# Kernel optimization log

Measured on AMD Instinct MI355X. Metric: run time of the kernel, lower is better.

## Reference

```python
import jax, jax.numpy as jnp
import numpy as np

B, S, T = 64, 512, 32
H2 = 1024          # hidden_size * 2
ATT = 512          # attention_size


def setup_inputs() -> dict:
    key = jax.random.key(0)
    k1, k2, k3, k4, k5, k6 = jax.random.split(key, 6)
    h = jax.random.normal(k1, (B, S, H2), dtype=jnp.float32)
    h_mask = jax.random.randint(k2, (B, S), 0, 2).astype(jnp.int32)
    ht = jax.random.normal(k3, (B, T, H2), dtype=jnp.float32)
    # Linear params (xavier-ish scale)
    w1_w = jax.random.normal(k4, (ATT, 2 * H2), dtype=jnp.float32) * (1.0 / np.sqrt(2 * H2))
    w1_b = jax.random.normal(k5, (ATT,), dtype=jnp.float32) * 0.02
    u_w = jax.random.normal(k6, (1, ATT), dtype=jnp.float32) * (1.0 / np.sqrt(ATT))
    return {"h": h, "h_mask": h_mask, "ht": ht, "w1_w": w1_w, "w1_b": w1_b, "u_w": u_w}


def reference(h, h_mask, ht, w1_w, w1_b, u_w):
    # h: [B,S,2H], ht: [B,T,2H], h_mask: [B,S] (1 = valid, 0 = pad)
    valid = h_mask != 0                                  # [B,S]
    ht_mean = jnp.mean(ht, axis=1, keepdims=True)        # [B,1,2H]
    h_cat = jnp.concatenate(
        [h, jnp.broadcast_to(ht_mean, h.shape)], axis=2)  # [B,S,4H]
    h_cat = jnp.where(valid[..., None], h_cat, 0.0)
    a = jnp.tanh(jnp.einsum('bsf,af->bsa', h_cat, w1_w) + w1_b)  # [B,S,ATT]
    a = jnp.where(valid[..., None], a, 0.0)
    beta = jnp.einsum('bsa,a->bs', a, u_w[0])            # [B,S]
    beta = jnp.where(valid, beta, -1e20)
    alpha = jax.nn.softmax(beta, axis=1)                 # [B,S]
    s = jnp.einsum('bs,bsd->bd', alpha, h)               # [B,2H]
    return s
```

## Files before the change

### kernel.cpp

```cpp
#include <hip/hip_runtime.h>
#include <math.h>
#include <stdint.h>

#define Bb 64
#define Ss 512
#define Tt 32
#define H2 1024
#define FF 2048
#define ATT 512
#define MM (Bb * Ss)

#define BM 64
#define BN 512
#define BK 32

typedef short bf8 __attribute__((ext_vector_type(8)));
typedef short bf4 __attribute__((ext_vector_type(4)));
typedef float f4 __attribute__((ext_vector_type(4)));

__device__ __forceinline__ unsigned short f2bf(float f) {
    unsigned u = __float_as_uint(f);
    u = (u + 0x7fffu + ((u >> 16) & 1u)) >> 16;
    return (unsigned short)u;
}

__device__ __forceinline__ void gl_lds16(const void* g, void* l) {
    __builtin_amdgcn_global_load_lds((const __attribute__((address_space(1))) void*)g,
                                     (__attribute__((address_space(3))) void*)l, 16, 0, 0);
}

__device__ __forceinline__ float tanh_fast(float x) {
    return 1.0f - 2.0f / (__expf(2.0f * x) + 1.0f);
}

__global__ void init_kernel(float* __restrict__ out) {
    int i = blockIdx.x * 256 + threadIdx.x;
    out[i] = 0.0f;
}

__global__ void mean_kernel(const float* __restrict__ ht, float* __restrict__ ht_mean) {
    int b = blockIdx.x;
    int d4 = threadIdx.x;
    const float4* p = (const float4*)(ht + (size_t)b * Tt * H2);
    float4 acc = make_float4(0.f, 0.f, 0.f, 0.f);
    #pragma unroll 4
    for (int t = 0; t < Tt; ++t) {
        float4 v = p[(size_t)t * (H2 / 4) + d4];
        acc.x += v.x; acc.y += v.y; acc.z += v.z; acc.w += v.w;
    }
    const float inv = 1.0f / (float)Tt;
    acc.x *= inv; acc.y *= inv; acc.z *= inv; acc.w *= inv;
    ((float4*)(ht_mean + (size_t)b * H2))[d4] = acc;
}

__global__ __launch_bounds__(256) void c2_kernel2(const float* __restrict__ ht_mean,
                                                  const float* __restrict__ w1_w,
                                                  const float* __restrict__ w1_b,
                                                  float* __restrict__ c2) {
    __shared__ float hm[H2];
    int b = blockIdx.x;
    for (int i = threadIdx.x; i < H2; i += 256) hm[i] = ht_mean[(size_t)b * H2 + i];
    __syncthreads();
    int a = blockIdx.y * 64 + ((int)threadIdx.x >> 2);
    int q = (int)threadIdx.x & 3;
    const float4* w   = (const float4*)(w1_w + (size_t)a * FF + H2 + q * 256);
    const float4* hm4 = (const float4*)(hm + q * 256);
    float acc = 0.f;
    #pragma unroll 8
    for (int k = 0; k < 64; ++k) {
        float4 wv = w[k]; float4 hv = hm4[k];
        acc += wv.x * hv.x + wv.y * hv.y + wv.z * hv.z + wv.w * hv.w;
    }
    acc += __shfl_xor(acc, 1);
    acc += __shfl_xor(acc, 2);
    if (q == 0) c2[(size_t)b * ATT + a] = acc + w1_b[a];
}

__global__ void convw_kernel(const float* __restrict__ w1_w, unsigned short* __restrict__ out) {
    size_t e = ((size_t)blockIdx.x * 256 + threadIdx.x) * 8;
    int row = (int)(e >> 10);
    int c = (int)(e & 1023);
    const float* src = w1_w + (size_t)row * FF + c;
    float4 a = *(const float4*)(src);
    float4 b = *(const float4*)(src + 4);
    bf8 v = { (short)f2bf(a.x), (short)f2bf(a.y), (short)f2bf(a.z), (short)f2bf(a.w),
              (short)f2bf(b.x), (short)f2bf(b.y), (short)f2bf(b.z), (short)f2bf(b.w) };
    *(bf8*)(out + e) = v;
}

__global__ __launch_bounds__(512, 4) void gemm_fused2_kernel(
        const float* __restrict__ h, const unsigned short* __restrict__ wb,
        const float* __restrict__ c2, const float* __restrict__ u_w,
        float* __restrict__ beta) {
    __shared__ __align__(16) unsigned short As[2][BM * BK];
    __shared__ __align__(16) unsigned short Bs[2][BN * BK];
    __shared__ float red[8][64];

    const int tid = (int)threadIdx.x;
    const int m0 = blockIdx.x * BM;
    const int wid = tid >> 6, lane = tid & 63;
    const int col = lane & 15, rg = lane >> 4;
    const int rswz = rg ^ ((col >> 1) & 3);

    f4 acc[4][4] = {};

    const int arow = tid >> 3;
    const int asub = tid & 7;
    const int a_elem = arow * BK + ((((asub >> 1) ^ ((arow >> 1) & 3)) * 8) + (asub & 1) * 4);
    const float* Ag = h + (size_t)(m0 + arow) * H2 + asub * 4;

    const int brow = tid >> 2;
    const int bslot_src = (tid & 3) ^ ((tid >> 3) & 3);
    const int ldsbase = wid * 512;

    #pragma unroll
    for (int c = 0; c < 4; ++c)
        gl_lds16(wb + (size_t)(c * 128 + brow) * H2 + bslot_src * 8,
                 &Bs[0][ldsbase + c * 4096]);
    {
        float4 a4 = *(const float4*)(Ag);
        bf4 ab = { (short)f2bf(a4.x), (short)f2bf(a4.y), (short)f2bf(a4.z), (short)f2bf(a4.w) };
        *(bf4*)&As[0][a_elem] = ab;
    }
    __syncthreads();

    int cur = 0;
    for (int t = 0; t < 32; ++t) {
        float4 a4n;
        if (t < 31) {
            a4n = *(const float4*)(Ag + (t + 1) * BK);
            #pragma unroll
            for (int c = 0; c < 4; ++c)
                gl_lds16(wb + (size_t)(c * 128 + brow) * H2 + (t + 1) * BK + bslot_src * 8,
                         &Bs[cur ^ 1][ldsbase + c * 4096]);
        }
        bf8 av[4], bv[4];
        #pragma unroll
        for (int i = 0; i < 4; ++i) {
            av[i] = *(const bf8*)&As[cur][(i * 16 + col) * BK + rswz * 8];
            bv[i] = *(const bf8*)&Bs[cur][(wid * 64 + i * 16 + col) * BK + rswz * 8];
        }
        #pragma unroll
        for (int i = 0; i < 4; ++i)
            #pragma unroll
            for (int j = 0; j < 4; ++j)
                acc[i][j] = __builtin_amdgcn_mfma_f32_16x16x32_bf16(av[i], bv[j], acc[i][j], 0, 0, 0);
        if (t < 31) {
            bf4 ab = { (short)f2bf(a4n.x), (short)f2bf(a4n.y), (short)f2bf(a4n.z), (short)f2bf(a4n.w) };
            *(bf4*)&As[cur ^ 1][a_elem] = ab;
        }
        __syncthreads();
        cur ^= 1;
    }

    const int b_idx = blockIdx.x >> 3;
    const float* c2b = c2 + (size_t)b_idx * ATT + wid * 64;
    const float* ub  = u_w + wid * 64;
    float rp[4][4] = {};
    #pragma unroll
    for (int j = 0; j < 4; ++j) {
        int n = j * 16 + col;
        float cv = c2b[n];
        float uv = ub[n];
        #pragma unroll
        for (int i = 0; i < 4; ++i)
            #pragma unroll
            for (int r = 0; r < 4; ++r)
                rp[i][r] += tanh_fast(acc[i][j][r] + cv) * uv;
    }
    #pragma unroll
    for (int i = 0; i < 4; ++i)
        #pragma unroll
        for (int r = 0; r < 4; ++r) {
            float v = rp[i][r];
            v += __shfl_xor(v, 1);
            v += __shfl_xor(v, 2);
            v += __shfl_xor(v, 4);
            v += __shfl_xor(v, 8);
            if (col == 0) red[wid][i * 16 + rg * 4 + r] = v;
        }
    __syncthreads();
    if (tid < 64) {
        float s = 0.f;
        #pragma unroll
        for (int w = 0; w < 8; ++w) s += red[w][tid];
        beta[(size_t)m0 + tid] = s;
    }
}

__global__ void softmax_kernel(const float* __restrict__ beta, const int* __restrict__ h_mask,
                               float* __restrict__ alpha) {
    __shared__ float red[16];
    int b = blockIdx.x;
    int s = (int)threadIdx.x;
    float v = (h_mask[(size_t)b * Ss + s] != 0) ? beta[(size_t)b * Ss + s] : -1e20f;
    float m = v;
    #pragma unroll
    for (int off = 32; off >= 1; off >>= 1) m = fmaxf(m, __shfl_xor(m, off, 64));
    int wave = s >> 6;
    if ((s & 63) == 0) red[wave] = m;
    __syncthreads();
    float mx = red[0];
    #pragma unroll
    for (int w = 1; w < 8; ++w) mx = fmaxf(mx, red[w]);
    float e = expf(v - mx);
    float sum = e;
    #pragma unroll
    for (int off = 32; off >= 1; off >>= 1) sum += __shfl_xor(sum, off, 64);
    __syncthreads();
    if ((s & 63) == 0) red[8 + wave] = sum;
    __syncthreads();
    float tot = 0.f;
    #pragma unroll
    for (int w = 0; w < 8; ++w) tot += red[8 + w];
    alpha[(size_t)b * Ss + s] = e / tot;
}

__global__ void wsum_kernel(const float* __restrict__ h, const float* __restrict__ alpha,
                            float* __restrict__ out) {
    int b = blockIdx.x;
    int d = blockIdx.y * 256 + (int)threadIdx.x;
    int s0 = blockIdx.z * 128;
    const float* hp = h + (size_t)b * Ss * H2 + (size_t)s0 * H2 + d;
    const float* ap = alpha + (size_t)b * Ss + s0;
    float acc = 0.f;
    #pragma unroll 4
    for (int s = 0; s < 128; ++s) acc = fmaf(ap[s], hp[(size_t)s * H2], acc);
    atomicAdd(&out[(size_t)b * H2 + d], acc);
}

extern "C" void kernel_launch(void* const* d_in, const int* in_sizes, int n_in,
                              void* d_out, int out_size, void* d_ws, size_t ws_size,
                              hipStream_t stream) {
    const float* h      = (const float*)d_in[0];
    const int*   h_mask = (const int*)d_in[1];
    const float* ht     = (const float*)d_in[2];
    const float* w1_w   = (const float*)d_in[3];
    const float* w1_b   = (const float*)d_in[4];
    const float* u_w    = (const float*)d_in[5];
    float* out = (float*)d_out;

    float* ws      = (float*)d_ws;
    float* ht_mean = ws;
    float* c2      = ws + 65536;
    float* beta    = ws + 98304;
    float* alpha   = ws + 131072;
    unsigned short* w1a_bf = (unsigned short*)(ws + 164864);

    hipLaunchKernelGGL(init_kernel, dim3(Bb * H2 / 256), dim3(256), 0, stream, out);
    hipLaunchKernelGGL(mean_kernel, dim3(Bb), dim3(256), 0, stream, ht, ht_mean);
    hipLaunchKernelGGL(c2_kernel2, dim3(Bb, 8), dim3(256), 0, stream, ht_mean, w1_w, w1_b, c2);
    hipLaunchKernelGGL(convw_kernel, dim3(256), dim3(256), 0, stream, w1_w, w1a_bf);
    hipLaunchKernelGGL(gemm_fused2_kernel, dim3(MM / BM), dim3(512), 0, stream,
                       h, w1a_bf, c2, u_w, beta);
    hipLaunchKernelGGL(softmax_kernel, dim3(Bb), dim3(512), 0, stream, beta, h_mask, alpha);
    hipLaunchKernelGGL(wsum_kernel, dim3(Bb, H2 / 256, 4), dim3(256), 0, stream, h, alpha, out);
}
```

Measured before the change: 294.4 us.

## Retile fused GEMM to 128x128 tiles with split-N atomic beta reduction

Replaces the 64x512 row-block GEMM (512 threads) with 128x128 output tiles on 256 threads, splitting the attention dimension across 4 workgroups. It also remaps block IDs so the N-tiles of one M-tile are spread apart, and widens the A loads to 16 floats per thread. Per-tile partial beta sums are combined with global atomicAdd instead of an in-block shared reduction, and init_kernel now zeroes beta as well. The aim is better balance between A and B reuse and more workgroups for occupancy. The cost is that each h row tile is loaded and converted 4 times, and beta picks up atomic contention.

```diff
diff --git a/kernel.cpp b/kernel.cpp
--- a/kernel.cpp
+++ b/kernel.cpp
@@ -10,12 +10,7 @@
 #define ATT 512
 #define MM (Bb * Ss)
 
-#define BM 64
-#define BN 512
-#define BK 32
-
 typedef short bf8 __attribute__((ext_vector_type(8)));
-typedef short bf4 __attribute__((ext_vector_type(4)));
 typedef float f4 __attribute__((ext_vector_type(4)));
 
 __device__ __forceinline__ unsigned short f2bf(float f) {
@@ -33,9 +28,10 @@
     return 1.0f - 2.0f / (__expf(2.0f * x) + 1.0f);
 }
 
-__global__ void init_kernel(float* __restrict__ out) {
+__global__ void init_kernel(float* __restrict__ beta, float* __restrict__ out) {
     int i = blockIdx.x * 256 + threadIdx.x;
-    out[i] = 0.0f;
+    if (i < Bb * Ss) beta[i] = 0.0f;
+    if (i < Bb * H2) out[i] = 0.0f;
 }
 
 __global__ void mean_kernel(const float* __restrict__ ht, float* __restrict__ ht_mean) {
@@ -88,57 +84,71 @@
     *(bf8*)(out + e) = v;
 }
 
-__global__ __launch_bounds__(512, 4) void gemm_fused2_kernel(
+__global__ __launch_bounds__(256, 3) void gemm_fused3_kernel(
         const float* __restrict__ h, const unsigned short* __restrict__ wb,
         const float* __restrict__ c2, const float* __restrict__ u_w,
         float* __restrict__ beta) {
-    __shared__ __align__(16) unsigned short As[2][BM * BK];
-    __shared__ __align__(16) unsigned short Bs[2][BN * BK];
-    __shared__ float red[8][64];
+    __shared__ __align__(16) unsigned short As[2][128 * 32];
+    __shared__ __align__(16) unsigned short Bs[2][128 * 32];
+
+    const int id = (int)blockIdx.x;
+    const int wg = (id & 7) * 128 + (id >> 3);
+    const int mt = wg >> 2, nt = wg & 3;
+    const int m0 = mt * 128, n0 = nt * 128;
 
     const int tid = (int)threadIdx.x;
-    const int m0 = blockIdx.x * BM;
     const int wid = tid >> 6, lane = tid & 63;
+    const int wr = (wid >> 1) * 64, wc = (wid & 1) * 64;
     const int col = lane & 15, rg = lane >> 4;
     const int rswz = rg ^ ((col >> 1) & 3);
 
     f4 acc[4][4] = {};
 
-    const int arow = tid >> 3;
-    const int asub = tid & 7;
-    const int a_elem = arow * BK + ((((asub >> 1) ^ ((arow >> 1) & 3)) * 8) + (asub & 1) * 4);
-    const float* Ag = h + (size_t)(m0 + arow) * H2 + asub * 4;
+    const int arow = tid >> 1;
+    const int ako  = (tid & 1) * 2;
+    const int aswz = (arow >> 1) & 3;
+    const float* Ag = h + (size_t)(m0 + arow) * H2 + ako * 8;
+    const int a_off0 = arow * 32 + ((ako    ) ^ aswz) * 8;
+    const int a_off1 = arow * 32 + ((ako + 1) ^ aswz) * 8;
 
     const int brow = tid >> 2;
-    const int bslot_src = (tid & 3) ^ ((tid >> 3) & 3);
-    const int ldsbase = wid * 512;
-
-    #pragma unroll
-    for (int c = 0; c < 4; ++c)
-        gl_lds16(wb + (size_t)(c * 128 + brow) * H2 + bslot_src * 8,
-                 &Bs[0][ldsbase + c * 4096]);
+    const int bsrc = (tid & 3) ^ ((tid >> 3) & 3);
+    const unsigned short* Bg = wb + (size_t)(n0 + brow) * H2 + bsrc * 8;
+    const int b_ldsbase = wid * 512;
+
+    gl_lds16(Bg,                   &Bs[0][b_ldsbase]);
+    gl_lds16(Bg + (size_t)64 * H2, &Bs[0][b_ldsbase + 2048]);
     {
-        float4 a4 = *(const float4*)(Ag);
-        bf4 ab = { (short)f2bf(a4.x), (short)f2bf(a4.y), (short)f2bf(a4.z), (short)f2bf(a4.w) };
-        *(bf4*)&As[0][a_elem] = ab;
+        float4 q0 = *(const float4*)(Ag);
+        float4 q1 = *(const float4*)(Ag + 4);
+        float4 q2 = *(const float4*)(Ag + 8);
+        float4 q3 = *(const float4*)(Ag + 12);
+        bf8 c0 = { (short)f2bf(q0.x), (short)f2bf(q0.y), (short)f2bf(q0.z), (short)f2bf(q0.w),
+                   (short)f2bf(q1.x), (short)f2bf(q1.y), (short)f2bf(q1.z), (short)f2bf(q1.w) };
+        bf8 c1 = { (short)f2bf(q2.x), (short)f2bf(q2.y), (short)f2bf(q2.z), (short)f2bf(q2.w),
+                   (short)f2bf(q3.x), (short)f2bf(q3.y), (short)f2bf(q3.z), (short)f2bf(q3.w) };
+        *(bf8*)&As[0][a_off0] = c0;
+        *(bf8*)&As[0][a_off1] = c1;
     }
     __syncthreads();
 
     int cur = 0;
     for (int t = 0; t < 32; ++t) {
-        float4 a4n;
+        float4 q0, q1, q2, q3;
         if (t < 31) {
-            a4n = *(const float4*)(Ag + (t + 1) * BK);
-            #pragma unroll
-            for (int c = 0; c < 4; ++c)
-                gl_lds16(wb + (size_t)(c * 128 + brow) * H2 + (t + 1) * BK + bslot_src * 8,
-                         &Bs[cur ^ 1][ldsbase + c * 4096]);
+            const int kn = (t + 1) * 32;
+            gl_lds16(Bg + kn,                   &Bs[cur ^ 1][b_ldsbase]);
+            gl_lds16(Bg + kn + (size_t)64 * H2, &Bs[cur ^ 1][b_ldsbase + 2048]);
+            q0 = *(const float4*)(Ag + kn);
+            q1 = *(const float4*)(Ag + kn + 4);
+            q2 = *(const float4*)(Ag + kn + 8);
+            q3 = *(const float4*)(Ag + kn + 12);
         }
         bf8 av[4], bv[4];
         #pragma unroll
         for (int i = 0; i < 4; ++i) {
-            av[i] = *(const bf8*)&As[cur][(i * 16 + col) * BK + rswz * 8];
-            bv[i] = *(const bf8*)&Bs[cur][(wid * 64 + i * 16 + col) * BK + rswz * 8];
+            av[i] = *(const bf8*)&As[cur][(wr + i * 16 + col) * 32 + rswz * 8];
+            bv[i] = *(const bf8*)&Bs[cur][(wc + i * 16 + col) * 32 + rswz * 8];
         }
         #pragma unroll
         for (int i = 0; i < 4; ++i)
@@ -146,16 +156,20 @@
             for (int j = 0; j < 4; ++j)
                 acc[i][j] = __builtin_amdgcn_mfma_f32_16x16x32_bf16(av[i], bv[j], acc[i][j], 0, 0, 0);
         if (t < 31) {
-            bf4 ab = { (short)f2bf(a4n.x), (short)f2bf(a4n.y), (short)f2bf(a4n.z), (short)f2bf(a4n.w) };
-            *(bf4*)&As[cur ^ 1][a_elem] = ab;
+            bf8 c0 = { (short)f2bf(q0.x), (short)f2bf(q0.y), (short)f2bf(q0.z), (short)f2bf(q0.w),
+                       (short)f2bf(q1.x), (short)f2bf(q1.y), (short)f2bf(q1.z), (short)f2bf(q1.w) };
+            bf8 c1 = { (short)f2bf(q2.x), (short)f2bf(q2.y), (short)f2bf(q2.z), (short)f2bf(q2.w),
+                       (short)f2bf(q3.x), (short)f2bf(q3.y), (short)f2bf(q3.z), (short)f2bf(q3.w) };
+            *(bf8*)&As[cur ^ 1][a_off0] = c0;
+            *(bf8*)&As[cur ^ 1][a_off1] = c1;
         }
         __syncthreads();
         cur ^= 1;
     }
 
-    const int b_idx = blockIdx.x >> 3;
-    const float* c2b = c2 + (size_t)b_idx * ATT + wid * 64;
-    const float* ub  = u_w + wid * 64;
+    const int b_idx = mt >> 2;
+    const float* c2b = c2 + (size_t)b_idx * ATT + n0 + wc;
+    const float* ub  = u_w + n0 + wc;
     float rp[4][4] = {};
     #pragma unroll
     for (int j = 0; j < 4; ++j) {
@@ -177,15 +191,9 @@
             v += __shfl_xor(v, 2);
             v += __shfl_xor(v, 4);
             v += __shfl_xor(v, 8);
-            if (col == 0) red[wid][i * 16 + rg * 4 + r] = v;
-        }
-    __syncthreads();
-    if (tid < 64) {
-        float s = 0.f;
-        #pragma unroll
-        for (int w = 0; w < 8; ++w) s += red[w][tid];
-        beta[(size_t)m0 + tid] = s;
-    }
+            if (col == 0)
+                atomicAdd(&beta[(size_t)m0 + wr + i * 16 + rg * 4 + r], v);
+        }
 }
 
 __global__ void softmax_kernel(const float* __restrict__ beta, const int* __restrict__ h_mask,
@@ -247,11 +255,11 @@
     float* alpha   = ws + 131072;
     unsigned short* w1a_bf = (unsigned short*)(ws + 164864);
 
-    hipLaunchKernelGGL(init_kernel, dim3(Bb * H2 / 256), dim3(256), 0, stream, out);
+    hipLaunchKernelGGL(init_kernel, dim3(256), dim3(256), 0, stream, beta, out);
     hipLaunchKernelGGL(mean_kernel, dim3(Bb), dim3(256), 0, stream, ht, ht_mean);
     hipLaunchKernelGGL(c2_kernel2, dim3(Bb, 8), dim3(256), 0, stream, ht_mean, w1_w, w1_b, c2);
     hipLaunchKernelGGL(convw_kernel, dim3(256), dim3(256), 0, stream, w1_w, w1a_bf);
-    hipLaunchKernelGGL(gemm_fused2_kernel, dim3(MM / BM), dim3(512), 0, stream,
+    hipLaunchKernelGGL(gemm_fused3_kernel, dim3((MM / 128) * (ATT / 128)), dim3(256), 0, stream,
                        h, w1a_bf, c2, u_w, beta);
     hipLaunchKernelGGL(softmax_kernel, dim3(Bb), dim3(512), 0, stream, beta, h_mask, alpha);
     hipLaunchKernelGGL(wsum_kernel, dim3(Bb, H2 / 256, 4), dim3(256), 0, stream, h, alpha, out);
```

Result: slower. 301.8 us (+2.5%).
